# Performance work log

Hardware: AMD Instinct MI355X
Metric: run time of the kernel (lower is better)

## Reference

```python
import jax, jax.numpy as jnp
import numpy as np

B, N, C = 4, 1024, 512
HEADS, DIM_HEAD = 8, 64
DIM_E, DIM_S, DIM_H = 64, 64, 32
INNER = HEADS * DIM_HEAD


def setup_inputs() -> dict:
    key = jax.random.key(0)
    ks = jax.random.split(key, 10)
    s = 0.02
    return {
        "x": jax.random.normal(ks[0], (B, N, C), jnp.float32),
        "w_qkv": jax.random.normal(ks[1], (3 * INNER, C), jnp.float32) * s,
        "w_proj": jax.random.normal(ks[2], (C, INNER), jnp.float32) * s,
        "b_proj": jnp.zeros((C,), jnp.float32),
        "w_e": jax.random.normal(ks[3], (DIM_E, DIM_HEAD), jnp.float32) * s,
        "b_e": jax.random.normal(ks[4], (DIM_E,), jnp.float32) * s,
        "w_s": jax.random.normal(ks[5], (DIM_S, DIM_HEAD), jnp.float32) * s,
        "b_s": jax.random.normal(ks[6], (DIM_S,), jnp.float32) * s,
        "w_h": jax.random.normal(ks[7], (DIM_H, DIM_HEAD), jnp.float32) * s,
        "b_h": jax.random.normal(ks[8], (DIM_H,), jnp.float32) * s,
        "alpha": jnp.float32(1.0),
        "beta": jnp.float32(1.0),
        "gamma": jnp.float32(1.0),
        "temperature": jnp.float32(1.0),
    }


def _sqdist(a, b):
    # |a_n - b_m|^2 via expansion; a,b: (B,H,N,d) -> (B,H,N,N)
    an = jnp.sum(a * a, -1)
    bn = jnp.sum(b * b, -1)
    return an[..., :, None] + bn[..., None, :] - 2.0 * jnp.einsum("bhnd,bhmd->bhnm", a, b)


def reference(x, w_qkv, w_proj, b_proj, w_e, b_e, w_s, b_s, w_h, b_h,
              alpha, beta, gamma, temperature):
    Bx, Nx, Cx = x.shape
    dh = w_e.shape[1]
    H = (w_qkv.shape[0] // 3) // dh

    qkv = x @ w_qkv.T                      # (B,N,3*inner)
    q, k, v = jnp.split(qkv, 3, axis=-1)
    to_heads = lambda t: t.reshape(Bx, Nx, H, dh).transpose(0, 2, 1, 3)  # (B,H,N,dh)
    q, k, v = to_heads(q), to_heads(k), to_heads(v)

    # metric embeddings
    eq, ek = q @ w_e.T + b_e, k @ w_e.T + b_e
    sq, sk = q @ w_s.T + b_s, k @ w_s.T + b_s
    sq = sq / jnp.maximum(jnp.linalg.norm(sq, axis=-1, keepdims=True), 1e-12)
    sk = sk / jnp.maximum(jnp.linalg.norm(sk, axis=-1, keepdims=True), 1e-12)
    hq, hk = jnp.tanh(q @ w_h.T + b_h), jnp.tanh(k @ w_h.T + b_h)

    # Euclidean (torch.cdist p=2)
    dE = jnp.sqrt(jnp.maximum(_sqdist(eq, ek), 1e-12))
    # spherical
    sim = jnp.einsum("bhnd,bhmd->bhnm", sq, sk)
    dS = jnp.arccos(jnp.clip(sim, -1.0 + 1e-6, 1.0 - 1e-6))
    # Poincare: diff_norm_sq expanded instead of (B,H,N,N,dim_h) broadcast tensor
    un = jnp.sum(hq * hq, -1)              # (B,H,N)
    vn = jnp.sum(hk * hk, -1)
    dns = jnp.maximum(_sqdist(hq, hk), 0.0)
    denom = (1.0 - un)[..., :, None] * (1.0 - vn)[..., None, :]
    arg = jnp.maximum(1.0 + 2.0 * dns / (denom + 1e-8), 1.0 + 1e-6)
    dH = jnp.arccosh(arg)

    sp = jax.nn.softplus
    D = sp(alpha) * dE + sp(beta) * dS + sp(gamma) * dH
    attn = jax.nn.softmax(-D / sp(temperature), axis=-1)  # (B,H,N,N)

    out = jnp.einsum("bhnm,bhmd->bhnd", attn, v)
    out = out.transpose(0, 2, 1, 3).reshape(Bx, Nx, H * dh)
    return out @ w_proj.T + b_proj
```

## Files before the change

### kernel.cpp

```cpp
#include <hip/hip_runtime.h>
#include <math.h>

typedef unsigned short u16;
typedef __attribute__((ext_vector_type(8))) short short8;
typedef __attribute__((ext_vector_type(4))) short short4v;
typedef __attribute__((ext_vector_type(4))) float floatx4;

#define BB 4
#define NN 1024
#define CC 512
#define HH 8
#define INNERD 512
#define BHCNT 32
#define MTOK 4096
#define NSPLIT 2

constexpr size_t OFF_XB  = 0;
constexpr size_t OFF_WQB = 4194304;
constexpr size_t OFF_WPB = 5767168;
constexpr size_t OFF_WEB = 6291456;
constexpr size_t OFF_WSB = 6299648;
constexpr size_t OFF_WHB = 6307840;
constexpr size_t OFF_QKV = 6311936;
constexpr size_t OFF_EQ  = 18894848;
constexpr size_t OFF_EK  = 23089152;
constexpr size_t OFF_SQ  = 27283456;
constexpr size_t OFF_SK  = 31477760;
constexpr size_t OFF_HQ  = 35672064;
constexpr size_t OFF_HK  = 37769216;
constexpr size_t OFF_VT  = 39866368;
constexpr size_t OFF_EQN = 44060672;
constexpr size_t OFF_EKN = 44191744;
constexpr size_t OFF_HQN = 44322816;
constexpr size_t OFF_HKN = 44453888;
constexpr size_t OFF_AO  = 44584960;
constexpr size_t OFF_OP  = 48779264;
constexpr size_t OFF_LP  = 65556480;

#if __has_builtin(__builtin_amdgcn_exp2f)
#define FEXP2(x) __builtin_amdgcn_exp2f(x)
#else
#define FEXP2(x) exp2f(x)
#endif
#if __has_builtin(__builtin_amdgcn_logf)
#define FLOG2(x) __builtin_amdgcn_logf(x)
#else
#define FLOG2(x) log2f(x)
#endif
#if __has_builtin(__builtin_amdgcn_sqrtf)
#define FSQRT(x) __builtin_amdgcn_sqrtf(x)
#else
#define FSQRT(x) sqrtf(x)
#endif
#if __has_builtin(__builtin_amdgcn_rcpf)
#define FRCP(x) __builtin_amdgcn_rcpf(x)
#else
#define FRCP(x) (1.0f / (x))
#endif

__device__ __forceinline__ short f2bf(float f) {
    unsigned u = __float_as_uint(f);
    unsigned r = u + 0x7fffu + ((u >> 16) & 1u);
    return (short)(r >> 16);
}
__device__ __forceinline__ floatx4 mfma16(short8 a, short8 b, floatx4 c) {
    return __builtin_amdgcn_mfma_f32_16x16x32_bf16(a, b, c, 0, 0, 0);
}
__device__ __forceinline__ float softplusf(float x) { return log1pf(expf(x)); }
__device__ __forceinline__ float qsum16(float v) {
    v += __shfl_xor(v, 1); v += __shfl_xor(v, 2);
    v += __shfl_xor(v, 4); v += __shfl_xor(v, 8);
    return v;
}
__device__ __forceinline__ float ftanh(float x) {
    const float t = FEXP2(x * 2.8853900817779268f);
    return (t - 1.0f) * FRCP(t + 1.0f);
}

__global__ __launch_bounds__(256) void k0_cvt(
    const float* __restrict__ x, const float* __restrict__ wq,
    const float* __restrict__ wp, const float* __restrict__ we,
    const float* __restrict__ wsp, const float* __restrict__ whp,
    u16* __restrict__ xb, u16* __restrict__ wqb, u16* __restrict__ wpb,
    u16* __restrict__ web, u16* __restrict__ wsb, u16* __restrict__ whb) {
    const size_t i = ((size_t)blockIdx.x * 256 + threadIdx.x) * 4;
    const float* s; u16* d; size_t off;
    if (i < 2097152)      { s = x;   d = xb;  off = i; }
    else if (i < 2883584) { s = wq;  d = wqb; off = i - 2097152; }
    else if (i < 3145728) { s = wp;  d = wpb; off = i - 2883584; }
    else if (i < 3149824) { s = we;  d = web; off = i - 3145728; }
    else if (i < 3153920) { s = wsp; d = wsb; off = i - 3149824; }
    else                  { s = whp; d = whb; off = i - 3153920; }
    const float4 v = *(const float4*)(s + off);
    short4v o;
    o[0] = f2bf(v.x); o[1] = f2bf(v.y); o[2] = f2bf(v.z); o[3] = f2bf(v.w);
    *(short4v*)(d + off) = o;
}

__global__ __launch_bounds__(256) void k1_qkv(const u16* __restrict__ x,
                                              const u16* __restrict__ wqkv,
                                              u16* __restrict__ qkv) {
    __shared__ u16 sB[2][64 * 40];
    const int tm = blockIdx.x * 64;
    const int o0 = blockIdx.y * 64;
    const int tid = threadIdx.x, lane = tid & 63, w = tid >> 6;
    const int l15 = lane & 15, quad = lane >> 4;
    const int arow = tm + w * 16 + l15;
    const int brow = tid >> 2, bj = (tid & 3) * 8;
    const int bOff = brow * 40 + bj;
    const u16* bsrc = wqkv + (size_t)(o0 + brow) * CC + bj;

    floatx4 acc[4];
    #pragma unroll
    for (int s = 0; s < 4; ++s) acc[s] = (floatx4){0.f, 0.f, 0.f, 0.f};

    *(short8*)&sB[0][bOff] = *(const short8*)bsrc;
    __syncthreads();

    #pragma unroll 1
    for (int kc = 0; kc < CC / 32; ++kc) {
        const int cur = kc & 1, nxt = cur ^ 1;
        short8 pB;
        if (kc + 1 < CC / 32) pB = *(const short8*)(bsrc + (kc + 1) * 32);

        short8 a = *(const short8*)(x + (size_t)arow * CC + kc * 32 + quad * 8);
        #pragma unroll
        for (int s = 0; s < 4; ++s) {
            short8 b = *(const short8*)&sB[cur][(s * 16 + l15) * 40 + quad * 8];
            acc[s] = mfma16(a, b, acc[s]);
        }
        if (kc + 1 < CC / 32) *(short8*)&sB[nxt][bOff] = pB;
        __syncthreads();
    }
    #pragma unroll
    for (int s = 0; s < 4; ++s) {
        const int o = o0 + s * 16 + l15;
        const int sq_i = o >> 9, rem = o & 511;
        const int h = rem >> 6, d = rem & 63;
        #pragma unroll
        for (int r = 0; r < 4; ++r) {
            const int tok = tm + w * 16 + quad * 4 + r;
            const int bb = tok >> 10, n = tok & (NN - 1);
            qkv[((((size_t)sq_i * BB + bb) * HH + h) * NN + n) * 64 + d] = (u16)f2bf(acc[s][r]);
        }
    }
}

__global__ __launch_bounds__(256) void k2_embed(
    const u16* __restrict__ qkv,
    const u16* __restrict__ we, const float* __restrict__ be,
    const u16* __restrict__ wsp, const float* __restrict__ bsp,
    const u16* __restrict__ whp, const float* __restrict__ bhp,
    u16* __restrict__ eq, u16* __restrict__ ek,
    u16* __restrict__ sq, u16* __restrict__ sk,
    u16* __restrict__ hq, u16* __restrict__ hk,
    float* __restrict__ eqn, float* __restrict__ ekn,
    float* __restrict__ hqn, float* __restrict__ hkn,
    u16* __restrict__ vt) {
    const int bh = blockIdx.x, n0 = blockIdx.y * 64;
    const int b = bh >> 3, h = bh & 7;
    const int tid = threadIdx.x, lane = tid & 63, w = tid >> 6;
    const int l15 = lane & 15, quad = lane >> 4;

    __shared__ u16 stg[64][72];
    const int srow = tid >> 2;
    const int scol = (tid & 3) * 16;

    for (int src = 0; src < 2; ++src) {
        const u16* qbase = qkv + (((size_t)src * BB + b) * HH + h) * NN * 64;
        const int tokA = n0 + w * 16 + l15;
        short8 afr[2];
        #pragma unroll
        for (int c = 0; c < 2; ++c)
            afr[c] = *(const short8*)(qbase + (size_t)tokA * 64 + c * 32 + quad * 8);

        floatx4 ce[4], cs[4], ch[2];
        #pragma unroll
        for (int i = 0; i < 4; ++i) { ce[i] = (floatx4){0.f,0.f,0.f,0.f}; cs[i] = (floatx4){0.f,0.f,0.f,0.f}; }
        #pragma unroll
        for (int i = 0; i < 2; ++i) ch[i] = (floatx4){0.f,0.f,0.f,0.f};

        #pragma unroll
        for (int c = 0; c < 2; ++c) {
            const int k0 = c * 32 + quad * 8;
            #pragma unroll
            for (int i = 0; i < 4; ++i) {
                short8 bf = *(const short8*)(we + (size_t)(i * 16 + l15) * 64 + k0);
                ce[i] = mfma16(afr[c], bf, ce[i]);
            }
            #pragma unroll
            for (int i = 0; i < 4; ++i) {
                short8 bf = *(const short8*)(wsp + (size_t)(i * 16 + l15) * 64 + k0);
                cs[i] = mfma16(afr[c], bf, cs[i]);
            }
            #pragma unroll
            for (int i = 0; i < 2; ++i) {
                short8 bf = *(const short8*)(whp + (size_t)(i * 16 + l15) * 64 + k0);
                ch[i] = mfma16(afr[c], bf, ch[i]);
            }
        }
        u16* edst = src ? ek : eq;
        u16* sdst = src ? sk : sq;
        u16* hdst = src ? hk : hq;
        float* endst = src ? ekn : eqn;
        float* hndst = src ? hkn : hqn;
        const int myrow = w * 16 + quad * 4;

        float epart[4] = {0.f, 0.f, 0.f, 0.f};
        #pragma unroll
        for (int i = 0; i < 4; ++i) {
            const float bias = be[i * 16 + l15];
            #pragma unroll
            for (int r = 0; r < 4; ++r) {
                const float v = ce[i][r] + bias;
                const short vb = f2bf(v);
                const float vr = __uint_as_float(((unsigned)(u16)vb) << 16);
                epart[r] += vr * vr;
                stg[myrow + r][i * 16 + l15] = (u16)vb;
            }
        }
        #pragma unroll
        for (int r = 0; r < 4; ++r) {
            const float s = qsum16(epart[r]);
            if (l15 == 0) endst[(size_t)bh * NN + n0 + myrow + r] = s;
        }
        __syncthreads();
        {
            short8 v0 = *(const short8*)&stg[srow][scol];
            short8 v1 = *(const short8*)&stg[srow][scol + 8];
            u16* dp = edst + ((size_t)bh * NN + n0 + srow) * 64 + scol;
            *(short8*)dp = v0;
            *(short8*)(dp + 8) = v1;
        }
        __syncthreads();

        float sv[4][4], sn2[4] = {0.f, 0.f, 0.f, 0.f};
        #pragma unroll
        for (int i = 0; i < 4; ++i) {
            const float bias = bsp[i * 16 + l15];
            #pragma unroll
            for (int r = 0; r < 4; ++r) {
                const float v = cs[i][r] + bias;
                sv[i][r] = v;
                sn2[r] += v * v;
            }
        }
        float inv[4];
        #pragma unroll
        for (int r = 0; r < 4; ++r) {
            const float t = qsum16(sn2[r]);
            inv[r] = FRCP(fmaxf(FSQRT(t), 1e-12f));
        }
        #pragma unroll
        for (int i = 0; i < 4; ++i) {
            #pragma unroll
            for (int r = 0; r < 4; ++r)
                stg[myrow + r][i * 16 + l15] = (u16)f2bf(sv[i][r] * inv[r]);
        }
        __syncthreads();
        {
            short8 v0 = *(const short8*)&stg[srow][scol];
            short8 v1 = *(const short8*)&stg[srow][scol + 8];
            u16* dp = sdst + ((size_t)bh * NN + n0 + srow) * 64 + scol;
            *(short8*)dp = v0;
            *(short8*)(dp + 8) = v1;
        }
        __syncthreads();

        float hpart[4] = {0.f, 0.f, 0.f, 0.f};
        #pragma unroll
        for (int i = 0; i < 2; ++i) {
            const float bias = bhp[i * 16 + l15];
            #pragma unroll
            for (int r = 0; r < 4; ++r) {
                const float v = ftanh(ch[i][r] + bias);
                const short vb = f2bf(v);
                const float vr = __uint_as_float(((unsigned)(u16)vb) << 16);
                hpart[r] += vr * vr;
                stg[myrow + r][i * 16 + l15] = (u16)vb;
            }
        }
        #pragma unroll
        for (int r = 0; r < 4; ++r) {
            const float s = qsum16(hpart[r]);
            if (l15 == 0) hndst[(size_t)bh * NN + n0 + myrow + r] = s;
        }
        __syncthreads();
        {
            const int hcol = (tid & 3) * 8;
            short8 v0 = *(const short8*)&stg[srow][hcol];
            u16* dp = hdst + ((size_t)bh * NN + n0 + srow) * 32 + hcol;
            *(short8*)dp = v0;
        }
        __syncthreads();
    }

    {
        const u16* vbase = qkv + (((size_t)2 * BB + b) * HH + h) * NN * 64;
        const u16* p = vbase + (size_t)(n0 + srow) * 64 + scol;
        *(short8*)(&stg[srow][scol]) = *(const short8*)p;
        *(short8*)(&stg[srow][scol + 8]) = *(const short8*)(p + 8);
    }
    __syncthreads();
    {
        const int d = tid >> 2, nn0 = (tid & 3) * 16;
        short8 o1, o2;
        #pragma unroll
        for (int j = 0; j < 8; ++j) o1[j] = (short)stg[nn0 + j][d];
        #pragma unroll
        for (int j = 0; j < 8; ++j) o2[j] = (short)stg[nn0 + 8 + j][d];
        u16* dst = vt + ((size_t)bh * 64 + d) * NN + n0 + nn0;
        *(short8*)dst = o1;
        *(short8*)(dst + 8) = o2;
    }
}

__global__ __launch_bounds__(256, 2) void k3_attn(
    const u16* __restrict__ eq, const u16* __restrict__ ek,
    const u16* __restrict__ sq, const u16* __restrict__ sk,
    const u16* __restrict__ hq, const u16* __restrict__ hk,
    const float* __restrict__ eqn, const float* __restrict__ ekn,
    const float* __restrict__ hqn, const float* __restrict__ hkn,
    const u16* __restrict__ vt,
    float* __restrict__ opart, float* __restrict__ lpart,
    const float* __restrict__ pA, const float* __restrict__ pB,
    const float* __restrict__ pG, const float* __restrict__ pT) {
    __shared__ u16 sE[32 * 72];
    __shared__ u16 sS[32 * 72];
    __shared__ u16 sH[32 * 40];
    __shared__ u16 sV[64 * 40];
    __shared__ float sEN[32];
    __shared__ float sHN[32];
    __shared__ u16 plds[4][2][16][36];

    const int bh = blockIdx.x, q0b = blockIdx.y * 128, split = blockIdx.z;
    const int tid = threadIdx.x, lane = tid & 63, w = tid >> 6;
    const int l15 = lane & 15, quad = lane >> 4;
    const int q0 = q0b + w * 16;

    const float invT = 1.0f / softplusf(pT[0]);
    const float L2E = 1.4426950408889634f;
    const float kE = -softplusf(pA[0]) * invT * L2E;
    const float kS = -softplusf(pB[0]) * invT * L2E;
    const float kH2 = -softplusf(pG[0]) * invT;

    const u16* ekb = ek + (size_t)bh * NN * 64;
    const u16* skb = sk + (size_t)bh * NN * 64;
    const u16* hkb = hk + (size_t)bh * NN * 32;
    const u16* vtb = vt + (size_t)bh * 64 * NN;
    const float* eknb = ekn + (size_t)bh * NN;
    const float* hknb = hkn + (size_t)bh * NN;

    const int kt0 = split * (NN / 32 / NSPLIT);
    const int ktend = kt0 + NN / 32 / NSPLIT;
    const int mbase = kt0 * 32;

    const int eKey = tid >> 3, eJ = (tid & 7) * 8;
    const int hKey = tid >> 2, hJ = (tid & 3) * 8;
    const int vD   = tid >> 2, vJ = (tid & 3) * 8;
    const int eOff = eKey * 72 + eJ;
    const int hOff = hKey * 40 + hJ;
    const int vOff = vD * 40 + vJ;

    short8 Ea[2][2], Sa[2][2], Ha[2];
    #pragma unroll
    for (int qt = 0; qt < 2; ++qt) {
        const size_t qrow = (size_t)bh * NN + q0 + qt * 64 + l15;
        #pragma unroll
        for (int c = 0; c < 2; ++c) {
            Ea[qt][c] = *(const short8*)(eq + qrow * 64 + c * 32 + quad * 8);
            Sa[qt][c] = *(const short8*)(sq + qrow * 64 + c * 32 + quad * 8);
        }
        Ha[qt] = *(const short8*)(hq + qrow * 32 + quad * 8);
    }

    float eqn_q[2][4], hqn_q[2][4], invcq[2][4];
    #pragma unroll
    for (int qt = 0; qt < 2; ++qt) {
        #pragma unroll
        for (int r = 0; r < 4; ++r) {
            const int t = q0 + qt * 64 + quad * 4 + r;
            eqn_q[qt][r] = eqn[(size_t)bh * NN + t];
            hqn_q[qt][r] = hqn[(size_t)bh * NN + t];
            invcq[qt][r] = FRCP(1.0f - hqn_q[qt][r]);
        }
    }

    {
        short8 vE = *(const short8*)(ekb + (size_t)(mbase + eKey) * 64 + eJ);
        short8 vS = *(const short8*)(skb + (size_t)(mbase + eKey) * 64 + eJ);
        short8 vV = *(const short8*)(vtb + (size_t)vD * NN + mbase + vJ);
        *(short8*)&sE[eOff] = vE;
        *(short8*)&sS[eOff] = vS;
        *(short8*)&sV[vOff] = vV;
        if (tid < 128) {
            short8 vH = *(const short8*)(hkb + (size_t)(mbase + hKey) * 32 + hJ);
            *(short8*)&sH[hOff] = vH;
        } else if (tid < 136) {
            float4 vN = *(const float4*)(eknb + mbase + (tid - 128) * 4);
            *(float4*)&sEN[(tid - 128) * 4] = vN;
        } else if (tid < 144) {
            float4 vN = *(const float4*)(hknb + mbase + (tid - 136) * 4);
            *(float4*)&sHN[(tid - 136) * 4] = vN;
        }
        __syncthreads();
    }

    floatx4 oacc[2][4];
    #pragma unroll
    for (int qt = 0; qt < 2; ++qt)
        #pragma unroll
        for (int db = 0; db < 4; ++db) oacc[qt][db] = (floatx4){0.f, 0.f, 0.f, 0.f};
    float lsum[2][4] = {{0.f, 0.f, 0.f, 0.f}, {0.f, 0.f, 0.f, 0.f}};

    const float PI_F = 3.14159265358979f;

    #pragma unroll 1
    for (int kt = kt0; kt < ktend; ++kt) {
        const bool more = (kt + 1 < ktend);

        short8 pE, pS, pV, pH;
        float4 pEN, pHN;
        if (more) {
            const int m0 = (kt + 1) * 32;
            pE = *(const short8*)(ekb + (size_t)(m0 + eKey) * 64 + eJ);
            pS = *(const short8*)(skb + (size_t)(m0 + eKey) * 64 + eJ);
            pV = *(const short8*)(vtb + (size_t)vD * NN + m0 + vJ);
            if (tid < 128) {
                pH = *(const short8*)(hkb + (size_t)(m0 + hKey) * 32 + hJ);
            } else if (tid < 136) {
                pEN = *(const float4*)(eknb + m0 + (tid - 128) * 4);
            } else if (tid < 144) {
                pHN = *(const float4*)(hknb + m0 + (tid - 136) * 4);
            }
        }

        #pragma unroll
        for (int sub = 0; sub < 2; ++sub) {
            const int row = sub * 16 + l15;
            short8 Eb0 = *(const short8*)&sE[row * 72 + quad * 8];
            short8 Eb1 = *(const short8*)&sE[row * 72 + 32 + quad * 8];
            short8 Sb0 = *(const short8*)&sS[row * 72 + quad * 8];
            short8 Sb1 = *(const short8*)&sS[row * 72 + 32 + quad * 8];
            short8 Hb  = *(const short8*)&sH[row * 40 + quad * 8];

            const float ekn_m = sEN[row];
            const float hkn_m = sHN[row];
            const float rck = FRCP(1.0f - hkn_m);
            const float rck2 = rck + rck;

            #pragma unroll
            for (int qt = 0; qt < 2; ++qt) {
                floatx4 z = (floatx4){0.f, 0.f, 0.f, 0.f};
                floatx4 se = mfma16(Ea[qt][1], Eb1, mfma16(Ea[qt][0], Eb0, z));
                floatx4 ss = mfma16(Sa[qt][1], Sb1, mfma16(Sa[qt][0], Sb0, z));
                floatx4 sh = mfma16(Ha[qt], Hb, z);

                #pragma unroll
                for (int r = 0; r < 4; ++r) {
                    const float dE = FSQRT(fmaxf(fmaf(se[r], -2.0f, eqn_q[qt][r] + ekn_m), 1e-12f));
                    const float t = fminf(fabsf(ss[r]), 0.999999f);
                    const float pol = fmaf(fmaf(fmaf(-0.0187293f, t, 0.0742610f), t,
                                                -0.2121144f), t, 1.5707288f);
                    const float rr = FSQRT(1.0f - t) * pol;
                    const float dS = (ss[r] >= 0.0f) ? rr : (PI_F - rr);
                    const float dns = fmaxf(fmaf(sh[r], -2.0f, hqn_q[qt][r] + hkn_m), 0.0f);
                    const float arg = fmaxf(fmaf(dns * invcq[qt][r], rck2, 1.0f), 1.0f + 1e-6f);
                    const float xs = arg + FSQRT(fmaf(arg, arg, -1.0f));
                    const float lgH = FLOG2(xs);
                    const float lg2 = fmaf(dE, kE, fmaf(dS, kS, lgH * kH2));
                    const float p = FEXP2(lg2);
                    const unsigned u = __float_as_uint(p);
                    lsum[qt][r] += __uint_as_float(u & 0xffff0000u);
                    plds[w][qt][quad * 4 + r][sub * 16 + l15] = (u16)(u >> 16);
                }
            }
        }
        short8 Vb[4];
        #pragma unroll
        for (int db = 0; db < 4; ++db)
            Vb[db] = *(const short8*)&sV[(db * 16 + l15) * 40 + quad * 8];
        #pragma unroll
        for (int qt = 0; qt < 2; ++qt) {
            short8 Pa = *(const short8*)(&plds[w][qt][l15][quad * 8]);
            #pragma unroll
            for (int db = 0; db < 4; ++db)
                oacc[qt][db] = mfma16(Pa, Vb[db], oacc[qt][db]);
        }

        __syncthreads();
        if (more) {
            *(short8*)&sE[eOff] = pE;
            *(short8*)&sS[eOff] = pS;
            *(short8*)&sV[vOff] = pV;
            if (tid < 128) {
                *(short8*)&sH[hOff] = pH;
            } else if (tid < 136) {
                *(float4*)&sEN[(tid - 128) * 4] = pEN;
            } else if (tid < 144) {
                *(float4*)&sHN[(tid - 136) * 4] = pHN;
            }
        }
        __syncthreads();
    }

    float* obase = opart + ((size_t)split * BHCNT + bh) * NN * 64;
    #pragma unroll
    for (int qt = 0; qt < 2; ++qt) {
        #pragma unroll
        for (int db = 0; db < 4; ++db) {
            #pragma unroll
            for (int r = 0; r < 4; ++r) {
                const int t = q0 + qt * 64 + quad * 4 + r;
                obase[(size_t)t * 64 + db * 16 + l15] = oacc[qt][db][r];
            }
        }
        #pragma unroll
        for (int r = 0; r < 4; ++r) {
            const float s = qsum16(lsum[qt][r]);
            if (l15 == 0)
                lpart[((size_t)split * BHCNT + bh) * NN + q0 + qt * 64 + quad * 4 + r] = s;
        }
    }
}

__global__ __launch_bounds__(256) void k3r_reduce(
    const float* __restrict__ opart, const float* __restrict__ lpart,
    u16* __restrict__ ao) {
    const size_t gid = (size_t)blockIdx.x * 256 + threadIdx.x;
    const size_t base = gid * 4;
    const int token = (int)(base >> 6);
    const int d0 = (int)(base & 63);
    float4 acc = {0.f, 0.f, 0.f, 0.f};
    float ls = 0.f;
    #pragma unroll
    for (int s = 0; s < NSPLIT; ++s) {
        const float4 v = *(const float4*)(opart + ((size_t)s * BHCNT * NN + token) * 64 + d0);
        acc.x += v.x; acc.y += v.y; acc.z += v.z; acc.w += v.w;
        ls += lpart[(size_t)s * BHCNT * NN + token];
    }
    const float inv = FRCP(ls);
    const int bh = token >> 10, n = token & (NN - 1);
    const int b = bh >> 3, h = bh & 7;
    short4v o;
    o[0] = f2bf(acc.x * inv); o[1] = f2bf(acc.y * inv);
    o[2] = f2bf(acc.z * inv); o[3] = f2bf(acc.w * inv);
    *(short4v*)(ao + ((size_t)b * NN + n) * INNERD + h * 64 + d0) = o;
}

__global__ __launch_bounds__(256) void k4_proj(const u16* __restrict__ ao,
                                               const u16* __restrict__ wp,
                                               const float* __restrict__ bp,
                                               float* __restrict__ out) {
    __shared__ u16 sB[2][64 * 40];
    const int tm = blockIdx.x * 64;
    const int o0 = blockIdx.y * 64;
    const int tid = threadIdx.x, lane = tid & 63, w = tid >> 6;
    const int l15 = lane & 15, quad = lane >> 4;
    const int arow = tm + w * 16 + l15;
    const int brow = tid >> 2, bj = (tid & 3) * 8;
    const int bOff = brow * 40 + bj;
    const u16* bsrc = wp + (size_t)(o0 + brow) * INNERD + bj;

    floatx4 acc[4];
    #pragma unroll
    for (int s = 0; s < 4; ++s) acc[s] = (floatx4){0.f, 0.f, 0.f, 0.f};

    *(short8*)&sB[0][bOff] = *(const short8*)bsrc;
    __syncthreads();

    #pragma unroll 1
    for (int kc = 0; kc < INNERD / 32; ++kc) {
        const int cur = kc & 1, nxt = cur ^ 1;
        short8 pB;
        if (kc + 1 < INNERD / 32) pB = *(const short8*)(bsrc + (kc + 1) * 32);

        short8 a = *(const short8*)(ao + (size_t)arow * INNERD + kc * 32 + quad * 8);
        #pragma unroll
        for (int s = 0; s < 4; ++s) {
            short8 b = *(const short8*)&sB[cur][(s * 16 + l15) * 40 + quad * 8];
            acc[s] = mfma16(a, b, acc[s]);
        }
        if (kc + 1 < INNERD / 32) *(short8*)&sB[nxt][bOff] = pB;
        __syncthreads();
    }
    #pragma unroll
    for (int s = 0; s < 4; ++s) {
        const int o = o0 + s * 16 + l15;
        const float bias = bp[o];
        #pragma unroll
        for (int r = 0; r < 4; ++r) {
            const int tok = tm + w * 16 + quad * 4 + r;
            out[(size_t)tok * CC + o] = acc[s][r] + bias;
        }
    }
}

extern "C" void kernel_launch(void* const* d_in, const int* in_sizes, int n_in,
                              void* d_out, int out_size, void* d_ws, size_t ws_size,
                              hipStream_t stream) {
    const float* x     = (const float*)d_in[0];
    const float* wqkv  = (const float*)d_in[1];
    const float* wproj = (const float*)d_in[2];
    const float* bproj = (const float*)d_in[3];
    const float* we    = (const float*)d_in[4];
    const float* be    = (const float*)d_in[5];
    const float* wsp   = (const float*)d_in[6];
    const float* bsp   = (const float*)d_in[7];
    const float* whp   = (const float*)d_in[8];
    const float* bhp   = (const float*)d_in[9];
    const float* pA    = (const float*)d_in[10];
    const float* pB    = (const float*)d_in[11];
    const float* pG    = (const float*)d_in[12];
    const float* pT    = (const float*)d_in[13];

    char* ws = (char*)d_ws;
    u16* xb  = (u16*)(ws + OFF_XB);
    u16* wqb = (u16*)(ws + OFF_WQB);
    u16* wpb = (u16*)(ws + OFF_WPB);
    u16* web = (u16*)(ws + OFF_WEB);
    u16* wsb = (u16*)(ws + OFF_WSB);
    u16* whb = (u16*)(ws + OFF_WHB);
    u16* qkv = (u16*)(ws + OFF_QKV);
    u16* eq = (u16*)(ws + OFF_EQ);
    u16* ek = (u16*)(ws + OFF_EK);
    u16* sq = (u16*)(ws + OFF_SQ);
    u16* sk = (u16*)(ws + OFF_SK);
    u16* hq = (u16*)(ws + OFF_HQ);
    u16* hk = (u16*)(ws + OFF_HK);
    u16* vt = (u16*)(ws + OFF_VT);
    float* eqn = (float*)(ws + OFF_EQN);
    float* ekn = (float*)(ws + OFF_EKN);
    float* hqn = (float*)(ws + OFF_HQN);
    float* hkn = (float*)(ws + OFF_HKN);
    u16* ao = (u16*)(ws + OFF_AO);
    float* opart = (float*)(ws + OFF_OP);
    float* lpart = (float*)(ws + OFF_LP);

    k0_cvt<<<3082, 256, 0, stream>>>(x, wqkv, wproj, we, wsp, whp,
                                     xb, wqb, wpb, web, wsb, whb);
    k1_qkv<<<dim3(MTOK / 64, 1536 / 64), 256, 0, stream>>>(xb, wqb, qkv);
    k2_embed<<<dim3(BHCNT, NN / 64), 256, 0, stream>>>(
        qkv, web, be, wsb, bsp, whb, bhp,
        eq, ek, sq, sk, hq, hk, eqn, ekn, hqn, hkn, vt);
    k3_attn<<<dim3(BHCNT, NN / 128, NSPLIT), 256, 0, stream>>>(
        eq, ek, sq, sk, hq, hk, eqn, ekn, hqn, hkn, vt, opart, lpart,
        pA, pB, pG, pT);
    k3r_reduce<<<(BHCNT * NN * 64 / 4) / 256, 256, 0, stream>>>(opart, lpart, ao);
    k4_proj<<<dim3(MTOK / 64, CC / 64), 256, 0, stream>>>(ao, wpb, bproj, (float*)d_out);
}
```

Baseline: 193.8 us.

## Enlarge GEMM token tiles, batch embed staging writes, double-buffer attention key tiles

The QKV and output projection GEMMs now compute 128 tokens per block instead of 64, so each shared-memory weight tile feeds twice as many MFMAs. Grid size halves and accumulator registers double. The embed kernel uses three separate staging buffers and writes E, S and H out after a single barrier pair, which drops four syncthreads per source. The attention kernel double-buffers its key, value and norm tiles in LDS and removes one barrier per key tile, at the cost of twice the shared memory and possibly lower occupancy.

```diff
diff --git a/kernel.cpp b/kernel.cpp
--- a/kernel.cpp
+++ b/kernel.cpp
@@ -101,7 +101,7 @@
                                               const u16* __restrict__ wqkv,
                                               u16* __restrict__ qkv) {
     __shared__ u16 sB[2][64 * 40];
-    const int tm = blockIdx.x * 64;
+    const int tm = blockIdx.x * 128;
     const int o0 = blockIdx.y * 64;
     const int tid = threadIdx.x, lane = tid & 63, w = tid >> 6;
     const int l15 = lane & 15, quad = lane >> 4;
@@ -110,9 +110,11 @@
     const int bOff = brow * 40 + bj;
     const u16* bsrc = wqkv + (size_t)(o0 + brow) * CC + bj;
 
-    floatx4 acc[4];
-    #pragma unroll
-    for (int s = 0; s < 4; ++s) acc[s] = (floatx4){0.f, 0.f, 0.f, 0.f};
+    floatx4 acc[2][4];
+    #pragma unroll
+    for (int qt = 0; qt < 2; ++qt)
+        #pragma unroll
+        for (int s = 0; s < 4; ++s) acc[qt][s] = (floatx4){0.f, 0.f, 0.f, 0.f};
 
     *(short8*)&sB[0][bOff] = *(const short8*)bsrc;
     __syncthreads();
@@ -123,25 +125,31 @@
         short8 pB;
         if (kc + 1 < CC / 32) pB = *(const short8*)(bsrc + (kc + 1) * 32);
 
-        short8 a = *(const short8*)(x + (size_t)arow * CC + kc * 32 + quad * 8);
+        short8 a0 = *(const short8*)(x + (size_t)arow * CC + kc * 32 + quad * 8);
+        short8 a1 = *(const short8*)(x + (size_t)(arow + 64) * CC + kc * 32 + quad * 8);
         #pragma unroll
         for (int s = 0; s < 4; ++s) {
             short8 b = *(const short8*)&sB[cur][(s * 16 + l15) * 40 + quad * 8];
-            acc[s] = mfma16(a, b, acc[s]);
+            acc[0][s] = mfma16(a0, b, acc[0][s]);
+            acc[1][s] = mfma16(a1, b, acc[1][s]);
         }
         if (kc + 1 < CC / 32) *(short8*)&sB[nxt][bOff] = pB;
         __syncthreads();
     }
     #pragma unroll
-    for (int s = 0; s < 4; ++s) {
-        const int o = o0 + s * 16 + l15;
-        const int sq_i = o >> 9, rem = o & 511;
-        const int h = rem >> 6, d = rem & 63;
-        #pragma unroll
-        for (int r = 0; r < 4; ++r) {
-            const int tok = tm + w * 16 + quad * 4 + r;
-            const int bb = tok >> 10, n = tok & (NN - 1);
-            qkv[((((size_t)sq_i * BB + bb) * HH + h) * NN + n) * 64 + d] = (u16)f2bf(acc[s][r]);
+    for (int qt = 0; qt < 2; ++qt) {
+        #pragma unroll
+        for (int s = 0; s < 4; ++s) {
+            const int o = o0 + s * 16 + l15;
+            const int sq_i = o >> 9, rem = o & 511;
+            const int h = rem >> 6, d = rem & 63;
+            #pragma unroll
+            for (int r = 0; r < 4; ++r) {
+                const int tok = tm + qt * 64 + w * 16 + quad * 4 + r;
+                const int bb = tok >> 10, n = tok & (NN - 1);
+                qkv[((((size_t)sq_i * BB + bb) * HH + h) * NN + n) * 64 + d] =
+                    (u16)f2bf(acc[qt][s][r]);
+            }
         }
     }
 }
@@ -162,9 +170,12 @@
     const int tid = threadIdx.x, lane = tid & 63, w = tid >> 6;
     const int l15 = lane & 15, quad = lane >> 4;
 
-    __shared__ u16 stg[64][72];
+    __shared__ u16 stgE[64][72];
+    __shared__ u16 stgS[64][72];
+    __shared__ u16 stgH[64][40];
     const int srow = tid >> 2;
     const int scol = (tid & 3) * 16;
+    const int hcol = (tid & 3) * 8;
 
     for (int src = 0; src < 2; ++src) {
         const u16* qbase = qkv + (((size_t)src * BB + b) * HH + h) * NN * 64;
@@ -216,7 +227,7 @@
                 const short vb = f2bf(v);
                 const float vr = __uint_as_float(((unsigned)(u16)vb) << 16);
                 epart[r] += vr * vr;
-                stg[myrow + r][i * 16 + l15] = (u16)vb;
+                stgE[myrow + r][i * 16 + l15] = (u16)vb;
             }
         }
         #pragma unroll
@@ -224,16 +235,6 @@
             const float s = qsum16(epart[r]);
             if (l15 == 0) endst[(size_t)bh * NN + n0 + myrow + r] = s;
         }
-        __syncthreads();
-        {
-            short8 v0 = *(const short8*)&stg[srow][scol];
-            short8 v1 = *(const short8*)&stg[srow][scol + 8];
-            u16* dp = edst + ((size_t)bh * NN + n0 + srow) * 64 + scol;
-            *(short8*)dp = v0;
-            *(short8*)(dp + 8) = v1;
-        }
-        __syncthreads();
-
         float sv[4][4], sn2[4] = {0.f, 0.f, 0.f, 0.f};
         #pragma unroll
         for (int i = 0; i < 4; ++i) {
@@ -255,18 +256,8 @@
         for (int i = 0; i < 4; ++i) {
             #pragma unroll
             for (int r = 0; r < 4; ++r)
-                stg[myrow + r][i * 16 + l15] = (u16)f2bf(sv[i][r] * inv[r]);
-        }
-        __syncthreads();
-        {
-            short8 v0 = *(const short8*)&stg[srow][scol];
-            short8 v1 = *(const short8*)&stg[srow][scol + 8];
-            u16* dp = sdst + ((size_t)bh * NN + n0 + srow) * 64 + scol;
-            *(short8*)dp = v0;
-            *(short8*)(dp + 8) = v1;
-        }
-        __syncthreads();
-
+                stgS[myrow + r][i * 16 + l15] = (u16)f2bf(sv[i][r] * inv[r]);
+        }
         float hpart[4] = {0.f, 0.f, 0.f, 0.f};
         #pragma unroll
         for (int i = 0; i < 2; ++i) {
@@ -277,7 +268,7 @@
                 const short vb = f2bf(v);
                 const float vr = __uint_as_float(((unsigned)(u16)vb) << 16);
                 hpart[r] += vr * vr;
-                stg[myrow + r][i * 16 + l15] = (u16)vb;
+                stgH[myrow + r][i * 16 + l15] = (u16)vb;
             }
         }
         #pragma unroll
@@ -287,10 +278,14 @@
         }
         __syncthreads();
         {
-            const int hcol = (tid & 3) * 8;
-            short8 v0 = *(const short8*)&stg[srow][hcol];
-            u16* dp = hdst + ((size_t)bh * NN + n0 + srow) * 32 + hcol;
-            *(short8*)dp = v0;
+            u16* dpE = edst + ((size_t)bh * NN + n0 + srow) * 64 + scol;
+            *(short8*)dpE = *(const short8*)&stgE[srow][scol];
+            *(short8*)(dpE + 8) = *(const short8*)&stgE[srow][scol + 8];
+            u16* dpS = sdst + ((size_t)bh * NN + n0 + srow) * 64 + scol;
+            *(short8*)dpS = *(const short8*)&stgS[srow][scol];
+            *(short8*)(dpS + 8) = *(const short8*)&stgS[srow][scol + 8];
+            u16* dpH = hdst + ((size_t)bh * NN + n0 + srow) * 32 + hcol;
+            *(short8*)dpH = *(const short8*)&stgH[srow][hcol];
         }
         __syncthreads();
     }
@@ -298,17 +293,17 @@
     {
         const u16* vbase = qkv + (((size_t)2 * BB + b) * HH + h) * NN * 64;
         const u16* p = vbase + (size_t)(n0 + srow) * 64 + scol;
-        *(short8*)(&stg[srow][scol]) = *(const short8*)p;
-        *(short8*)(&stg[srow][scol + 8]) = *(const short8*)(p + 8);
+        *(short8*)(&stgE[srow][scol]) = *(const short8*)p;
+        *(short8*)(&stgE[srow][scol + 8]) = *(const short8*)(p + 8);
     }
     __syncthreads();
     {
         const int d = tid >> 2, nn0 = (tid & 3) * 16;
         short8 o1, o2;
         #pragma unroll
-        for (int j = 0; j < 8; ++j) o1[j] = (short)stg[nn0 + j][d];
-        #pragma unroll
-        for (int j = 0; j < 8; ++j) o2[j] = (short)stg[nn0 + 8 + j][d];
+        for (int j = 0; j < 8; ++j) o1[j] = (short)stgE[nn0 + j][d];
+        #pragma unroll
+        for (int j = 0; j < 8; ++j) o2[j] = (short)stgE[nn0 + 8 + j][d];
         u16* dst = vt + ((size_t)bh * 64 + d) * NN + n0 + nn0;
         *(short8*)dst = o1;
         *(short8*)(dst + 8) = o2;
@@ -325,12 +320,12 @@
     float* __restrict__ opart, float* __restrict__ lpart,
     const float* __restrict__ pA, const float* __restrict__ pB,
     const float* __restrict__ pG, const float* __restrict__ pT) {
-    __shared__ u16 sE[32 * 72];
-    __shared__ u16 sS[32 * 72];
-    __shared__ u16 sH[32 * 40];
-    __shared__ u16 sV[64 * 40];
-    __shared__ float sEN[32];
-    __shared__ float sHN[32];
+    __shared__ u16 sE[2][32 * 72];
+    __shared__ u16 sS[2][32 * 72];
+    __shared__ u16 sH[2][32 * 40];
+    __shared__ u16 sV[2][64 * 40];
+    __shared__ float sEN[2][32];
+    __shared__ float sHN[2][32];
     __shared__ u16 plds[4][2][16][36];
 
     const int bh = blockIdx.x, q0b = blockIdx.y * 128, split = blockIdx.z;
@@ -390,18 +385,18 @@
         short8 vE = *(const short8*)(ekb + (size_t)(mbase + eKey) * 64 + eJ);
         short8 vS = *(const short8*)(skb + (size_t)(mbase + eKey) * 64 + eJ);
         short8 vV = *(const short8*)(vtb + (size_t)vD * NN + mbase + vJ);
-        *(short8*)&sE[eOff] = vE;
-        *(short8*)&sS[eOff] = vS;
-        *(short8*)&sV[vOff] = vV;
+        *(short8*)&sE[0][eOff] = vE;
+        *(short8*)&sS[0][eOff] = vS;
+        *(short8*)&sV[0][vOff] = vV;
         if (tid < 128) {
             short8 vH = *(const short8*)(hkb + (size_t)(mbase + hKey) * 32 + hJ);
-            *(short8*)&sH[hOff] = vH;
+            *(short8*)&sH[0][hOff] = vH;
         } else if (tid < 136) {
             float4 vN = *(const float4*)(eknb + mbase + (tid - 128) * 4);
-            *(float4*)&sEN[(tid - 128) * 4] = vN;
+            *(float4*)&sEN[0][(tid - 128) * 4] = vN;
         } else if (tid < 144) {
             float4 vN = *(const float4*)(hknb + mbase + (tid - 136) * 4);
-            *(float4*)&sHN[(tid - 136) * 4] = vN;
+            *(float4*)&sHN[0][(tid - 136) * 4] = vN;
         }
         __syncthreads();
     }
@@ -417,6 +412,7 @@
 
     #pragma unroll 1
     for (int kt = kt0; kt < ktend; ++kt) {
+        const int cur = (kt - kt0) & 1, nxt = cur ^ 1;
         const bool more = (kt + 1 < ktend);
 
         short8 pE, pS, pV, pH;
@@ -438,14 +434,14 @@
         #pragma unroll
         for (int sub = 0; sub < 2; ++sub) {
             const int row = sub * 16 + l15;
-            short8 Eb0 = *(const short8*)&sE[row * 72 + quad * 8];
-            short8 Eb1 = *(const short8*)&sE[row * 72 + 32 + quad * 8];
-            short8 Sb0 = *(const short8*)&sS[row * 72 + quad * 8];
-            short8 Sb1 = *(const short8*)&sS[row * 72 + 32 + quad * 8];
-            short8 Hb  = *(const short8*)&sH[row * 40 + quad * 8];
-
-            const float ekn_m = sEN[row];
-            const float hkn_m = sHN[row];
+            short8 Eb0 = *(const short8*)&sE[cur][row * 72 + quad * 8];
+            short8 Eb1 = *(const short8*)&sE[cur][row * 72 + 32 + quad * 8];
+            short8 Sb0 = *(const short8*)&sS[cur][row * 72 + quad * 8];
+            short8 Sb1 = *(const short8*)&sS[cur][row * 72 + 32 + quad * 8];
+            short8 Hb  = *(const short8*)&sH[cur][row * 40 + quad * 8];
+
+            const float ekn_m = sEN[cur][row];
+            const float hkn_m = sHN[cur][row];
             const float rck = FRCP(1.0f - hkn_m);
             const float rck2 = rck + rck;
 
@@ -479,7 +475,7 @@
         short8 Vb[4];
         #pragma unroll
         for (int db = 0; db < 4; ++db)
-            Vb[db] = *(const short8*)&sV[(db * 16 + l15) * 40 + quad * 8];
+            Vb[db] = *(const short8*)&sV[cur][(db * 16 + l15) * 40 + quad * 8];
         #pragma unroll
         for (int qt = 0; qt < 2; ++qt) {
             short8 Pa = *(const short8*)(&plds[w][qt][l15][quad * 8]);
@@ -488,17 +484,16 @@
                 oacc[qt][db] = mfma16(Pa, Vb[db], oacc[qt][db]);
         }
 
-        __syncthreads();
         if (more) {
-            *(short8*)&sE[eOff] = pE;
-            *(short8*)&sS[eOff] = pS;
-            *(short8*)&sV[vOff] = pV;
+            *(short8*)&sE[nxt][eOff] = pE;
+            *(short8*)&sS[nxt][eOff] = pS;
+            *(short8*)&sV[nxt][vOff] = pV;
             if (tid < 128) {
-                *(short8*)&sH[hOff] = pH;
+                *(short8*)&sH[nxt][hOff] = pH;
             } else if (tid < 136) {
-                *(float4*)&sEN[(tid - 128) * 4] = pEN;
+                *(float4*)&sEN[nxt][(tid - 128) * 4] = pEN;
             } else if (tid < 144) {
-                *(float4*)&sHN[(tid - 136) * 4] = pHN;
+                *(float4*)&sHN[nxt][(tid - 136) * 4] = pHN;
             }
         }
         __syncthreads();
@@ -553,7 +548,7 @@
                                                const float* __restrict__ bp,
                                                float* __restrict__ out) {
     __shared__ u16 sB[2][64 * 40];
-    const int tm = blockIdx.x * 64;
+    const int tm = blockIdx.x * 128;
     const int o0 = blockIdx.y * 64;
     const int tid = threadIdx.x, lane = tid & 63, w = tid >> 6;
     const int l15 = lane & 15, quad = lane >> 4;
@@ -562,9 +557,11 @@
     const int bOff = brow * 40 + bj;
     const u16* bsrc = wp + (size_t)(o0 + brow) * INNERD + bj;
 
-    floatx4 acc[4];
-    #pragma unroll
-    for (int s = 0; s < 4; ++s) acc[s] = (floatx4){0.f, 0.f, 0.f, 0.f};
+    floatx4 acc[2][4];
+    #pragma unroll
+    for (int qt = 0; qt < 2; ++qt)
+        #pragma unroll
+        for (int s = 0; s < 4; ++s) acc[qt][s] = (floatx4){0.f, 0.f, 0.f, 0.f};
 
     *(short8*)&sB[0][bOff] = *(const short8*)bsrc;
     __syncthreads();
@@ -575,23 +572,28 @@
         short8 pB;
         if (kc + 1 < INNERD / 32) pB = *(const short8*)(bsrc + (kc + 1) * 32);
 
-        short8 a = *(const short8*)(ao + (size_t)arow * INNERD + kc * 32 + quad * 8);
+        short8 a0 = *(const short8*)(ao + (size_t)arow * INNERD + kc * 32 + quad * 8);
+        short8 a1 = *(const short8*)(ao + (size_t)(arow + 64) * INNERD + kc * 32 + quad * 8);
         #pragma unroll
         for (int s = 0; s < 4; ++s) {
             short8 b = *(const short8*)&sB[cur][(s * 16 + l15) * 40 + quad * 8];
-            acc[s] = mfma16(a, b, acc[s]);
+            acc[0][s] = mfma16(a0, b, acc[0][s]);
+            acc[1][s] = mfma16(a1, b, acc[1][s]);
         }
         if (kc + 1 < INNERD / 32) *(short8*)&sB[nxt][bOff] = pB;
         __syncthreads();
     }
     #pragma unroll
-    for (int s = 0; s < 4; ++s) {
-        const int o = o0 + s * 16 + l15;
-        const float bias = bp[o];
-        #pragma unroll
-        for (int r = 0; r < 4; ++r) {
-            const int tok = tm + w * 16 + quad * 4 + r;
-            out[(size_t)tok * CC + o] = acc[s][r] + bias;
+    for (int qt = 0; qt < 2; ++qt) {
+        #pragma unroll
+        for (int s = 0; s < 4; ++s) {
+            const int o = o0 + s * 16 + l15;
+            const float bias = bp[o];
+            #pragma unroll
+            for (int r = 0; r < 4; ++r) {
+                const int tok = tm + qt * 64 + w * 16 + quad * 4 + r;
+                out[(size_t)tok * CC + o] = acc[qt][s][r] + bias;
+            }
         }
     }
 }
@@ -639,7 +641,7 @@
 
     k0_cvt<<<3082, 256, 0, stream>>>(x, wqkv, wproj, we, wsp, whp,
                                      xb, wqb, wpb, web, wsb, whb);
-    k1_qkv<<<dim3(MTOK / 64, 1536 / 64), 256, 0, stream>>>(xb, wqb, qkv);
+    k1_qkv<<<dim3(MTOK / 128, 1536 / 64), 256, 0, stream>>>(xb, wqb, qkv);
     k2_embed<<<dim3(BHCNT, NN / 64), 256, 0, stream>>>(
         qkv, web, be, wsb, bsp, whb, bhp,
         eq, ek, sq, sk, hq, hk, eqn, ekn, hqn, hkn, vt);
@@ -647,5 +649,5 @@
         eq, ek, sq, sk, hq, hk, eqn, ekn, hqn, hkn, vt, opart, lpart,
         pA, pB, pG, pT);
     k3r_reduce<<<(BHCNT * NN * 64 / 4) / 256, 256, 0, stream>>>(opart, lpart, ao);
-    k4_proj<<<dim3(MTOK / 64, CC / 64), 256, 0, stream>>>(ao, wpb, bproj, (float*)d_out);
-}
+    k4_proj<<<dim3(MTOK / 128, CC / 64), 256, 0, stream>>>(ao, wpb, bproj, (float*)d_out);
+}
```

New measurement: 196.1 us. About the same (+1.2%).
